# Kernel tuning notes

Measured on AMD Instinct MI355X. Metric: run time of the kernel, lower is better.

Reference implementation:

```python
import jax, jax.numpy as jnp
import numpy as np


def euler2mat(angle):
    """angle: [..., 3] euler angles (x, y, z) -> [..., 3, 3] rotation matrix (xmat @ ymat @ zmat)."""
    x, y, z = angle[..., 0], angle[..., 1], angle[..., 2]
    zo = jnp.zeros_like(z)
    on = jnp.ones_like(z)
    cz, sz = jnp.cos(z), jnp.sin(z)
    cy, sy = jnp.cos(y), jnp.sin(y)
    cx, sx = jnp.cos(x), jnp.sin(x)
    zmat = jnp.stack([cz, -sz, zo, sz, cz, zo, zo, zo, on], axis=-1).reshape(*z.shape, 3, 3)
    ymat = jnp.stack([cy, zo, sy, zo, on, zo, -sy, zo, cy], axis=-1).reshape(*z.shape, 3, 3)
    xmat = jnp.stack([on, zo, zo, zo, cx, -sx, zo, sx, cx], axis=-1).reshape(*z.shape, 3, 3)
    return xmat @ ymat @ zmat


def pixel_grid(H, W, dtype=jnp.float32):
    """Matches torch affine_grid(identity, align_corners=False): normalized (x, y) in (-1, 1)."""
    xs = (2.0 * (jnp.arange(W, dtype=dtype) + 0.5) / W) - 1.0
    ys = (2.0 * (jnp.arange(H, dtype=dtype) + 0.5) / H) - 1.0
    X, Y = jnp.meshgrid(xs, ys, indexing='xy')  # [H, W] each
    return jnp.stack([X, Y], axis=-1)  # [H, W, 2], last dim = (x, y)


def setup_inputs() -> dict:
    key = jax.random.key(0)
    k1, k2, k3, k4, k5 = jax.random.split(key, 5)
    B, K, H, W = 8, 8, 384, 384
    im = jax.random.normal(k1, (B, H, W), dtype=jnp.float32)
    mask = jax.random.uniform(k2, (B, K, H, W), dtype=jnp.float32)
    depth = jax.random.uniform(k3, (B, H, W), dtype=jnp.float32, minval=0.5, maxval=1.5)
    T = jax.random.normal(k4, (B, K, 6), dtype=jnp.float32) * 0.1
    Tc = jax.random.normal(k5, (B, 9), dtype=jnp.float32) * 0.1
    return {"im": im, "mask": mask, "depth": depth, "T": T, "Tc": Tc}


def reference(im, mask, depth, T, Tc):
    B, K, H, W = mask.shape
    pixel = jnp.broadcast_to(pixel_grid(H, W, depth.dtype), (B, H, W, 2))  # [B,H,W,2]

    # object transforms
    t, a = T[..., 0:3], T[..., 3:6]            # [B,K,3] each
    R = euler2mat(a)                           # [B,K,3,3]
    # camera transform
    tc = Tc[..., 0:3]                          # [B,3]
    Rc = euler2mat(Tc[..., 3:6])               # [B,3,3]
    pc = Tc[..., 6:9]                          # [B,3]

    # pixel -> world (focal length = 1): [B,H,W,3]
    ones = jnp.ones((B, H, W, 1), dtype=depth.dtype)
    world = depth[..., None] * jnp.concatenate([pixel, ones], axis=-1)

    # centre of mass per mask: [B,K,3]
    total_mass = jnp.sum(mask, axis=(2, 3))[..., None] + 1e-6  # [B,K,1]
    p = jnp.einsum('bkhw,bhwc->bkc', mask, world) / total_mass

    # per-object rigid transform about centre of mass
    centered = world[:, None] - p[:, :, None, None]                       # [B,K,H,W,3]
    rotated = jnp.einsum('bkij,bkhwj->bkhwi', R, centered)                # [B,K,H,W,3]
    twc_k = rotated + (p + t)[:, :, None, None]                           # [B,K,H,W,3]

    # mask-weighted blend of per-object displacements
    twc = world + jnp.einsum('bkhw,bkhwc->bhwc', mask, twc_k - world[:, None])

    # camera transform about pivot pc
    twc = jnp.einsum('bij,bhwj->bhwi', Rc, twc - pc[:, None, None])
    twc = twc + (pc + tc)[:, None, None]

    # world -> pixel, flow
    new_pixel = twc[..., 0:2] / twc[..., 2:3]
    flow = new_pixel - pixel
    return flow
```

## Files before the change

kernel.cpp:

```cpp
#include <hip/hip_runtime.h>

#define B 8
#define K 8
#define H 384
#define W 384
#define HW (H*W)
#define NCPP 16
#define GROUPS_PER_B (HW/4)

typedef float f32x4 __attribute__((ext_vector_type(4)));

__device__ __forceinline__ float4 ntload4(const float* p) {
    f32x4 v = __builtin_nontemporal_load((const f32x4*)p);
    return make_float4(v.x, v.y, v.z, v.w);
}


__device__ __forceinline__ void euler2mat(float ax, float ay, float az, float R[9]) {
    float cx = cosf(ax), sx = sinf(ax);
    float cy = cosf(ay), sy = sinf(ay);
    float cz = cosf(az), sz = sinf(az);
    R[0] = cy*cz;              R[1] = -cy*sz;             R[2] = sy;
    R[3] = cx*sz + sx*sy*cz;   R[4] = cx*cz - sx*sy*sz;   R[5] = -sx*cy;
    R[6] = sx*sz - cx*sy*cz;   R[7] = sx*cz + cx*sy*sz;   R[8] = cx*cy;
}

__global__ __launch_bounds__(256) void k_reduce(const float* __restrict__ mask,
                                                const float* __restrict__ depth,
                                                float* __restrict__ ws) {
    const int chunk = blockIdx.x, k = blockIdx.y, b = blockIdx.z;
    const int tid = threadIdx.x;

    const float* mbase = mask + ((size_t)(b*K + k)) * HW;
    const float4* d4 = (const float4*)(depth + (size_t)b * HW);

    float s0 = 0.f, s1 = 0.f, s2 = 0.f, s3 = 0.f;
    const float inv = 2.f / W;

#pragma unroll
    for (int r = 0; r < 9; ++r) {
        int g = (chunk * 9 + r) * 256 + tid;
        float4 mv = ntload4(mbase + (size_t)g * 4);
        float4 dv = d4[g];
        int i0 = g * 4;
        int h = i0 / W;
        int w0 = i0 - h * W;
        float py = 2.f * (h + 0.5f) * (1.f / H) - 1.f;
        float px0 = 2.f * (w0 + 0.5f) * (1.f / W) - 1.f;
        float mm[4] = {mv.x, mv.y, mv.z, mv.w};
        float dd[4] = {dv.x, dv.y, dv.z, dv.w};
#pragma unroll
        for (int j = 0; j < 4; ++j) {
            float m = mm[j];
            float t = m * dd[j];
            float px = px0 + j * inv;
            s0 += m; s1 += t * px; s2 += t * py; s3 += t;
        }
    }

    for (int off = 32; off > 0; off >>= 1) {
        s0 += __shfl_down(s0, off);
        s1 += __shfl_down(s1, off);
        s2 += __shfl_down(s2, off);
        s3 += __shfl_down(s3, off);
    }
    __shared__ float sd[16];
    int lane = tid & 63, wid = tid >> 6;
    if (lane == 0) { sd[wid*4+0]=s0; sd[wid*4+1]=s1; sd[wid*4+2]=s2; sd[wid*4+3]=s3; }
    __syncthreads();
    if (tid < 4) {
        float v = sd[tid] + sd[4 + tid] + sd[8 + tid] + sd[12 + tid];
        ws[(((b*K + k) * NCPP) + chunk) * 4 + tid] = v;
    }
}

__global__ __launch_bounds__(256) void k_flow(const float* __restrict__ mask,
                                              const float* __restrict__ depth,
                                              const float* __restrict__ T,
                                              const float* __restrict__ Tc,
                                              const float* __restrict__ ws,
                                              float* __restrict__ out) {
    const int b = blockIdx.y;
    const int tid = threadIdx.x;

    __shared__ float sP[512];
    __shared__ float s32[32];
    __shared__ float sp[108];

    int g = blockIdx.x * 256 + tid;
    int i0 = g * 4;
    float4 dv = ((const float4*)(depth + (size_t)b * HW))[g];

    float4 mf[K];
#pragma unroll
    for (int k = 0; k < K; ++k) {
        mf[k] = ntload4(mask + ((size_t)(b*K + k)) * HW + (size_t)g * 4);
        asm volatile("s_waitcnt vmcnt(0)" ::: "memory");
    }

    if (tid < 128)
        ((float4*)sP)[tid] = ((const float4*)(ws + (size_t)b * 512))[tid];
    __syncthreads();

    if (tid < 32) {
        int k = tid >> 2, comp = tid & 3;
        float s = 0.f;
#pragma unroll
        for (int ch = 0; ch < NCPP; ++ch) s += sP[(k * NCPP + ch) * 4 + comp];
        s32[tid] = s;
    }
    __syncthreads();

    if (tid < 8) {
        int k = tid;
        float mass = s32[k*4 + 0] + 1e-6f;
        float p0 = s32[k*4 + 1] / mass;
        float p1 = s32[k*4 + 2] / mass;
        float p2 = s32[k*4 + 3] / mass;
        const float* Tk = T + (b*K + k) * 6;
        float R[9];
        euler2mat(Tk[3], Tk[4], Tk[5], R);
        float Rp0 = R[0]*p0 + R[1]*p1 + R[2]*p2;
        float Rp1 = R[3]*p0 + R[4]*p1 + R[5]*p2;
        float Rp2 = R[6]*p0 + R[7]*p1 + R[8]*p2;
        float* o = sp + k * 12;
        o[0] = R[0] - 1.f; o[1] = R[1];       o[2] = R[2];
        o[3] = R[3];       o[4] = R[4] - 1.f; o[5] = R[5];
        o[6] = R[6];       o[7] = R[7];       o[8] = R[8] - 1.f;
        o[9]  = p0 + Tk[0] - Rp0;
        o[10] = p1 + Tk[1] - Rp1;
        o[11] = p2 + Tk[2] - Rp2;
    } else if (tid == 8) {
        const float* Tb = Tc + b * 9;
        float R[9];
        euler2mat(Tb[3], Tb[4], Tb[5], R);
        float pc0 = Tb[6], pc1 = Tb[7], pc2 = Tb[8];
        float* o = sp + 96;
#pragma unroll
        for (int i = 0; i < 9; ++i) o[i] = R[i];
        o[9]  = pc0 + Tb[0] - (R[0]*pc0 + R[1]*pc1 + R[2]*pc2);
        o[10] = pc1 + Tb[1] - (R[3]*pc0 + R[4]*pc1 + R[5]*pc2);
        o[11] = pc2 + Tb[2] - (R[6]*pc0 + R[7]*pc1 + R[8]*pc2);
    }
    __syncthreads();

    int h = i0 / W;
    int w0 = i0 - h * W;
    float py = 2.f * (h + 0.5f) * (1.f / H) - 1.f;
    const float inv = 2.f / W;
    float px0 = 2.f * (w0 + 0.5f) * (1.f / W) - 1.f;

    float dd[4] = {dv.x, dv.y, dv.z, dv.w};
    float res[8];
#pragma unroll
    for (int j = 0; j < 4; ++j) {
        float px = px0 + j * inv;
        float d = dd[j];
        float wx = d * px, wy = d * py, wz = d;
        float ax = wx, ay = wy, az = wz;
#pragma unroll
        for (int k = 0; k < K; ++k) {
            const float* P = sp + k * 12;
            float m = (j == 0) ? mf[k].x : (j == 1) ? mf[k].y : (j == 2) ? mf[k].z : mf[k].w;
            float rx = P[0]*wx + P[1]*wy + P[2]*wz + P[9];
            float ry = P[3]*wx + P[4]*wy + P[5]*wz + P[10];
            float rz = P[6]*wx + P[7]*wy + P[8]*wz + P[11];
            ax += m * rx; ay += m * ry; az += m * rz;
        }
        const float* C = sp + 96;
        float ox = C[0]*ax + C[1]*ay + C[2]*az + C[9];
        float oy = C[3]*ax + C[4]*ay + C[5]*az + C[10];
        float oz = C[6]*ax + C[7]*ay + C[8]*az + C[11];
        res[j*2 + 0] = ox / oz - px;
        res[j*2 + 1] = oy / oz - py;
    }

    f32x4* o4 = (f32x4*)(out + ((size_t)b * HW + i0) * 2);
    f32x4 v0 = {res[0], res[1], res[2], res[3]};
    f32x4 v1 = {res[4], res[5], res[6], res[7]};
    __builtin_nontemporal_store(v0, o4);
    __builtin_nontemporal_store(v1, o4 + 1);
}

extern "C" void kernel_launch(void* const* d_in, const int* in_sizes, int n_in,
                              void* d_out, int out_size, void* d_ws, size_t ws_size,
                              hipStream_t stream) {
    const float* mask  = (const float*)d_in[1];
    const float* depth = (const float*)d_in[2];
    const float* T     = (const float*)d_in[3];
    const float* Tc    = (const float*)d_in[4];
    float* ws  = (float*)d_ws;
    float* out = (float*)d_out;

    k_reduce<<<dim3(NCPP, K, B), 256, 0, stream>>>(mask, depth, ws);
    k_flow<<<dim3(GROUPS_PER_B / 256, B), 256, 0, stream>>>(mask, depth, T, Tc, ws, out);
}
```

Baseline: 31.34 us.

## Transpose mask into interleaved workspace during reduction for contiguous flow reads

The reduction kernel now handles mask channels in pairs and also writes the mask into a workspace laid out so each pixel group's channels sit next to each other. The flow kernel then reads the mask from that interleaved copy with ordinary loads instead of eight strided nontemporal loads serialized by explicit waitcnt barriers. This adds a full extra write and read of the mask (about 37 MB of extra traffic) in exchange for better access locality and no serialization. It also halves the reduction grid.

```diff
diff --git a/kernel.cpp b/kernel.cpp
--- a/kernel.cpp
+++ b/kernel.cpp
@@ -7,6 +7,8 @@
 #define HW (H*W)
 #define NCPP 16
 #define GROUPS_PER_B (HW/4)
+#define MT_FLOATS ((size_t)B*4*GROUPS_PER_B*8)
+#define WSP_OFF MT_FLOATS
 
 typedef float f32x4 __attribute__((ext_vector_type(4)));
 
@@ -14,7 +16,6 @@
     f32x4 v = __builtin_nontemporal_load((const f32x4*)p);
     return make_float4(v.x, v.y, v.z, v.w);
 }
-
 
 __device__ __forceinline__ void euler2mat(float ax, float ay, float az, float R[9]) {
     float cx = cosf(ax), sx = sinf(ax);
@@ -25,61 +26,71 @@
     R[6] = sx*sz - cx*sy*cz;   R[7] = sx*cz + cx*sy*sz;   R[8] = cx*cy;
 }
 
-__global__ __launch_bounds__(256) void k_reduce(const float* __restrict__ mask,
-                                                const float* __restrict__ depth,
-                                                float* __restrict__ ws) {
-    const int chunk = blockIdx.x, k = blockIdx.y, b = blockIdx.z;
+__global__ __launch_bounds__(256) void k_trans(const float* __restrict__ mask,
+                                               const float* __restrict__ depth,
+                                               float* __restrict__ ws) {
+    const int chunk = blockIdx.x, kp = blockIdx.y, b = blockIdx.z;
     const int tid = threadIdx.x;
 
-    const float* mbase = mask + ((size_t)(b*K + k)) * HW;
+    const float* mA = mask + ((size_t)(b*K + 2*kp)) * HW;
+    const float* mB = mA + HW;
     const float4* d4 = (const float4*)(depth + (size_t)b * HW);
-
-    float s0 = 0.f, s1 = 0.f, s2 = 0.f, s3 = 0.f;
+    float4* mt = (float4*)ws + (size_t)(b*4 + kp) * GROUPS_PER_B * 2;
+
+    float a0=0.f,a1=0.f,a2=0.f,a3=0.f;
+    float c0=0.f,c1=0.f,c2=0.f,c3=0.f;
     const float inv = 2.f / W;
 
 #pragma unroll
     for (int r = 0; r < 9; ++r) {
         int g = (chunk * 9 + r) * 256 + tid;
-        float4 mv = ntload4(mbase + (size_t)g * 4);
+        float4 va = ntload4(mA + (size_t)g * 4);
+        float4 vb = ntload4(mB + (size_t)g * 4);
         float4 dv = d4[g];
         int i0 = g * 4;
         int h = i0 / W;
         int w0 = i0 - h * W;
         float py = 2.f * (h + 0.5f) * (1.f / H) - 1.f;
         float px0 = 2.f * (w0 + 0.5f) * (1.f / W) - 1.f;
-        float mm[4] = {mv.x, mv.y, mv.z, mv.w};
+        float ma[4] = {va.x, va.y, va.z, va.w};
+        float mb[4] = {vb.x, vb.y, vb.z, vb.w};
         float dd[4] = {dv.x, dv.y, dv.z, dv.w};
 #pragma unroll
         for (int j = 0; j < 4; ++j) {
-            float m = mm[j];
-            float t = m * dd[j];
             float px = px0 + j * inv;
-            s0 += m; s1 += t * px; s2 += t * py; s3 += t;
+            float t = ma[j] * dd[j];
+            a0 += ma[j]; a1 += t * px; a2 += t * py; a3 += t;
+            float u = mb[j] * dd[j];
+            c0 += mb[j]; c1 += u * px; c2 += u * py; c3 += u;
         }
+        mt[(size_t)g * 2 + 0] = va;
+        mt[(size_t)g * 2 + 1] = vb;
     }
 
     for (int off = 32; off > 0; off >>= 1) {
-        s0 += __shfl_down(s0, off);
-        s1 += __shfl_down(s1, off);
-        s2 += __shfl_down(s2, off);
-        s3 += __shfl_down(s3, off);
-    }
-    __shared__ float sd[16];
+        a0 += __shfl_down(a0, off); a1 += __shfl_down(a1, off);
+        a2 += __shfl_down(a2, off); a3 += __shfl_down(a3, off);
+        c0 += __shfl_down(c0, off); c1 += __shfl_down(c1, off);
+        c2 += __shfl_down(c2, off); c3 += __shfl_down(c3, off);
+    }
+    __shared__ float sd[32];
     int lane = tid & 63, wid = tid >> 6;
-    if (lane == 0) { sd[wid*4+0]=s0; sd[wid*4+1]=s1; sd[wid*4+2]=s2; sd[wid*4+3]=s3; }
-    __syncthreads();
-    if (tid < 4) {
-        float v = sd[tid] + sd[4 + tid] + sd[8 + tid] + sd[12 + tid];
-        ws[(((b*K + k) * NCPP) + chunk) * 4 + tid] = v;
-    }
-}
-
-__global__ __launch_bounds__(256) void k_flow(const float* __restrict__ mask,
-                                              const float* __restrict__ depth,
-                                              const float* __restrict__ T,
-                                              const float* __restrict__ Tc,
-                                              const float* __restrict__ ws,
-                                              float* __restrict__ out) {
+    if (lane == 0) {
+        sd[wid*8+0]=a0; sd[wid*8+1]=a1; sd[wid*8+2]=a2; sd[wid*8+3]=a3;
+        sd[wid*8+4]=c0; sd[wid*8+5]=c1; sd[wid*8+6]=c2; sd[wid*8+7]=c3;
+    }
+    __syncthreads();
+    if (tid < 8) {
+        float v = sd[tid] + sd[8 + tid] + sd[16 + tid] + sd[24 + tid];
+        ws[WSP_OFF + (((size_t)(b*4 + kp)) * NCPP + chunk) * 8 + tid] = v;
+    }
+}
+
+__global__ __launch_bounds__(256) void k_flow2(const float* __restrict__ depth,
+                                               const float* __restrict__ T,
+                                               const float* __restrict__ Tc,
+                                               const float* __restrict__ ws,
+                                               float* __restrict__ out) {
     const int b = blockIdx.y;
     const int tid = threadIdx.x;
 
@@ -87,26 +98,28 @@
     __shared__ float s32[32];
     __shared__ float sp[108];
 
-    int g = blockIdx.x * 256 + tid;
-    int i0 = g * 4;
+    const int g = blockIdx.x * 256 + tid;
+    const int i0 = g * 4;
     float4 dv = ((const float4*)(depth + (size_t)b * HW))[g];
 
-    float4 mf[K];
-#pragma unroll
-    for (int k = 0; k < K; ++k) {
-        mf[k] = ntload4(mask + ((size_t)(b*K + k)) * HW + (size_t)g * 4);
-        asm volatile("s_waitcnt vmcnt(0)" ::: "memory");
+    float4 pf[8];
+#pragma unroll
+    for (int kp = 0; kp < 4; ++kp) {
+        const float4* mt = (const float4*)ws + (size_t)(b*4 + kp) * GROUPS_PER_B * 2;
+        pf[kp*2 + 0] = mt[(size_t)g*2 + 0];
+        pf[kp*2 + 1] = mt[(size_t)g*2 + 1];
     }
 
     if (tid < 128)
-        ((float4*)sP)[tid] = ((const float4*)(ws + (size_t)b * 512))[tid];
+        ((float4*)sP)[tid] = ((const float4*)(ws + WSP_OFF + (size_t)b * 512))[tid];
     __syncthreads();
 
     if (tid < 32) {
         int k = tid >> 2, comp = tid & 3;
+        int kp = k >> 1, lsb = k & 1;
         float s = 0.f;
 #pragma unroll
-        for (int ch = 0; ch < NCPP; ++ch) s += sP[(k * NCPP + ch) * 4 + comp];
+        for (int ch = 0; ch < NCPP; ++ch) s += sP[kp*128 + ch*8 + lsb*4 + comp];
         s32[tid] = s;
     }
     __syncthreads();
@@ -161,7 +174,7 @@
 #pragma unroll
         for (int k = 0; k < K; ++k) {
             const float* P = sp + k * 12;
-            float m = (j == 0) ? mf[k].x : (j == 1) ? mf[k].y : (j == 2) ? mf[k].z : mf[k].w;
+            float m = (j == 0) ? pf[k].x : (j == 1) ? pf[k].y : (j == 2) ? pf[k].z : pf[k].w;
             float rx = P[0]*wx + P[1]*wy + P[2]*wz + P[9];
             float ry = P[3]*wx + P[4]*wy + P[5]*wz + P[10];
             float rz = P[6]*wx + P[7]*wy + P[8]*wz + P[11];
@@ -192,6 +205,6 @@
     float* ws  = (float*)d_ws;
     float* out = (float*)d_out;
 
-    k_reduce<<<dim3(NCPP, K, B), 256, 0, stream>>>(mask, depth, ws);
-    k_flow<<<dim3(GROUPS_PER_B / 256, B), 256, 0, stream>>>(mask, depth, T, Tc, ws, out);
-}
+    k_trans<<<dim3(NCPP, 4, B), 256, 0, stream>>>(mask, depth, ws);
+    k_flow2<<<dim3(GROUPS_PER_B / 256, B), 256, 0, stream>>>(depth, T, Tc, ws, out);
+}
```

New measurement: 37.76 us. +20.5%, slower.
